# Performance work log

Measured on AMD Instinct MI355X. Metric: run time of the kernel, lower is better.

The kernel has to match this reference:

```python
import jax, jax.numpy as jnp
import numpy as np

INV_SQRT2 = 0.7071067811865476


def _dense(x, W):
    return jax.nn.silu(x @ W)


def _residual(x, Wa, Wb):
    # GemNet ResidualLayer: two activated dense layers, skip, 1/sqrt(2) rescale
    return (x + _dense(_dense(x, Wa), Wb)) * INV_SQRT2


def setup_inputs() -> dict:
    key = jax.random.key(0)
    ks = iter(jax.random.split(key, 40))
    N, E, T = 10000, 200000, 400000
    NR, NS = 128, 7          # num_radial, num_spherical
    A, M, Ti, To, C = 128, 256, 64, 64, 16
    NB = 2                   # num_blocks

    def w(shape):
        fan_in = shape[-2]
        return jax.random.normal(next(ks), shape, jnp.float32) / float(np.sqrt(fan_in))

    inp = {}
    inp['atomic_numbers'] = jax.random.randint(next(ks), (N,), 0, 120)
    inp['idx_s'] = jax.random.randint(next(ks), (E,), 0, N)
    inp['idx_t'] = jax.random.randint(next(ks), (E,), 0, N)
    inp['id3_ba'] = jax.random.randint(next(ks), (T,), 0, E)
    inp['id3_ca'] = jax.random.randint(next(ks), (T,), 0, E)
    inp['rbf'] = jax.random.uniform(next(ks), (E, NR), jnp.float32)
    inp['cbf'] = jax.random.normal(next(ks), (T, NS), jnp.float32)
    V = jax.random.normal(next(ks), (E, 3), jnp.float32)
    inp['V_st'] = V / jnp.linalg.norm(V, axis=-1, keepdims=True)
    inp['atom_table'] = jax.random.normal(next(ks), (120, A), jnp.float32)
    inp['W_edge_in'] = w((2 * A + NR, M))
    inp['rbf_w3'] = w((NB, NR, M))
    inp['W_down'] = w((NB, M, Ti))
    inp['W_cbf'] = w((NB, NS, C))
    inp['W_bil'] = jax.random.normal(next(ks), (NB, C, Ti, To), jnp.float32) / float(np.sqrt(C * Ti))
    inp['W_up'] = w((NB, To, M))
    inp['W_res_e'] = w((NB, 4, M, M))
    inp['rbf_wh'] = w((NB, NR, M))
    inp['W_e2a'] = w((NB, M, A))
    inp['W_res_a'] = w((NB, 2, A, A))
    inp['W_outE_in'] = w((A * (NB + 1), A))
    inp['W_outE_res'] = w((2, A, A))
    inp['W_outE_fin'] = w((A, 1))
    inp['W_outF_in'] = w((M * (NB + 1), M))
    inp['W_outF_res'] = w((2, M, M))
    inp['W_outF_fin'] = w((M, 1))
    return inp


def reference(atomic_numbers, idx_s, idx_t, id3_ba, id3_ca, rbf, cbf, V_st,
              atom_table, W_edge_in, rbf_w3, W_down, W_cbf, W_bil, W_up,
              W_res_e, rbf_wh, W_e2a, W_res_a,
              W_outE_in, W_outE_res, W_outE_fin,
              W_outF_in, W_outF_res, W_outF_fin):
    N = atomic_numbers.shape[0]
    E = idx_s.shape[0]
    NB = rbf_w3.shape[0]

    # atom and edge embeddings
    h = atom_table[atomic_numbers]                                       # [N, A]
    m = _dense(jnp.concatenate([h[idx_s], h[idx_t], rbf], axis=-1), W_edge_in)  # [E, M]

    xs_E = [h]
    xs_F = [m]
    for b in range(NB):
        # --- triplet interaction: edge -> triplet gather, bilinear CBF mix, scatter back ---
        x = (m * (rbf @ rbf_w3[b])) @ W_down[b]                          # [E, Ti]
        cb = cbf @ W_cbf[b]                                              # [T, C]
        y = jnp.einsum('tc,ti,cio->to', cb, x[id3_ba], W_bil[b])         # [T, To]
        agg = jax.ops.segment_sum(y, id3_ca, num_segments=E)             # [E, To]
        x3 = _dense(agg @ W_up[b], jnp.eye(x3_dim := W_up[b].shape[1], dtype=m.dtype)) if False else jax.nn.silu(agg @ W_up[b])  # [E, M]
        # --- residual / skip structure ---
        m2 = _residual(m, W_res_e[b, 0], W_res_e[b, 1])
        m2 = (m2 + x3) * INV_SQRT2
        m = _residual(m2, W_res_e[b, 2], W_res_e[b, 3])
        # --- atom update: edge -> atom scatter ---
        xa = (m * (rbf @ rbf_wh[b])) @ W_e2a[b]                          # [E, A]
        ha = jax.ops.segment_sum(xa, idx_t, num_segments=N)              # [N, A]
        h = h + _residual(ha, W_res_a[b, 0], W_res_a[b, 1])
        xs_E.append(h)
        xs_F.append(m)

    # FinalMLP-style heads over concatenated per-block features (emb*(num_blocks+1))
    xE = _residual(_dense(jnp.concatenate(xs_E, axis=-1), W_outE_in), W_outE_res[0], W_outE_res[1])
    E_atom = xE @ W_outE_fin                                             # [N, 1]
    xF = _residual(_dense(jnp.concatenate(xs_F, axis=-1), W_outF_in), W_outF_res[0], W_outF_res[1])
    F_edge = xF @ W_outF_fin                                             # [E, 1]
    forces = jax.ops.segment_sum(F_edge * V_st, idx_t, num_segments=N)   # [N, 3]
    return jnp.concatenate([E_atom, forces], axis=-1)                    # [N, 4]
```

## Files before the change

### kernel.cpp

```cpp
#include <hip/hip_runtime.h>
#include <hip/hip_bf16.h>
#include <cstdio>

#define INV2 0.70710678118654752440f
typedef __hip_bfloat16 bf16;
typedef __attribute__((ext_vector_type(8))) short short8v;
typedef __attribute__((ext_vector_type(8))) unsigned short u16x8;
typedef __attribute__((ext_vector_type(4))) float f32x4;

__device__ __forceinline__ float silu_f(float v) { return v / (1.0f + __expf(-v)); }
__device__ __forceinline__ float bf2f(unsigned short u) {
    union { unsigned int i; float f; } t; t.i = ((unsigned int)u) << 16; return t.f;
}
__device__ __forceinline__ unsigned short f2bf(float x) {
    bf16 b = __float2bfloat16(x);
    return *reinterpret_cast<unsigned short*>(&b);
}
__device__ __forceinline__ float toF(float v) { return v; }
__device__ __forceinline__ float toF(bf16 v) { return __bfloat162float(v); }
__device__ __forceinline__ void stF(float* p, float v) { *p = v; }
__device__ __forceinline__ void stF(bf16* p, float v) { *p = __float2bfloat16(v); }

__device__ __forceinline__ void ld8f(const float* p, float* o) {
    const float4 a = ((const float4*)p)[0], b = ((const float4*)p)[1];
    o[0]=a.x; o[1]=a.y; o[2]=a.z; o[3]=a.w; o[4]=b.x; o[5]=b.y; o[6]=b.z; o[7]=b.w;
}
__device__ __forceinline__ void ld8f(const bf16* p, float* o) {
    const u16x8 u = *(const u16x8*)p;
#pragma unroll
    for (int j = 0; j < 8; j++) o[j] = bf2f(u[j]);
}

__device__ __forceinline__ void gll16(const void* g, void* l) {
    __builtin_amdgcn_global_load_lds(
        (const __attribute__((address_space(1))) unsigned int*)g,
        (__attribute__((address_space(3))) unsigned int*)l, 16, 0, 0);
}

enum { AM_NORMAL = 0, AM_MUL2 = 1, AM_GATHER = 2, AM_SILU = 3, AM_DMA = 4 };
enum { EP_PLAIN = 0, EP_SILU = 1, EP_ACCUM = 2, EP_RES2 = 3, EP_RESADD = 4, EP_HEADRES = 5 };

template <int AMODE, int EPI, int BN, typename AT, typename CT>
__global__ __launch_bounds__(256) void mgemm(
    const AT* __restrict__ A, const AT* __restrict__ A2,
    const int* __restrict__ gs, const int* __restrict__ gt,
    const bf16* __restrict__ Bt,
    CT* __restrict__ C, const CT* __restrict__ X,
    int Mrows, int Ncols, int K)
{
    constexpr bool DMA = (AMODE == AM_DMA);
    constexpr int AST = DMA ? 32 : 40;
    constexpr int FM = (BN == 128) ? 4 : 2;
    __shared__ __align__(16) unsigned short Als[128 * AST];
    __shared__ __align__(16) unsigned short Bls[BN * 32];
    const int tid = threadIdx.x;
    const int row0 = blockIdx.x * 128, col0 = blockIdx.y * BN;

    const int sr = tid >> 1;
    const int sh = (tid & 1) * 16;
    const int gr = row0 + sr;
    const bool rok = (gr < Mrows);
    int is_ = 0, it_ = 0;
    if (AMODE == AM_GATHER) { if (rok) { is_ = gs[gr]; it_ = gt[gr]; } }

    const int l = tid & 63, wid = tid >> 6;
    const int lr = l & 15;
    const int lk = (l >> 4) * 8;
    const int wrow = (BN == 128) ? ((wid & 1) * 64) : (wid * 32);
    const int wcol = (BN == 128) ? ((wid >> 1) * 64) : 0;

    f32x4 acc[FM][4];
#pragma unroll
    for (int i = 0; i < FM; i++)
#pragma unroll
        for (int j = 0; j < 4; j++)
#pragma unroll
            for (int q = 0; q < 4; q++) acc[i][j][q] = 0.f;

    for (int k0 = 0; k0 < K; k0 += 32) {
        if constexpr (DMA) {
#pragma unroll
            for (int i = 0; i < 2; i++) {
                const int c = i * 256 + tid;
                const int row = c >> 2;
                if (row0 + row < Mrows)
                    gll16(A + (size_t)(row0 + row) * K + k0 + (c & 3) * 8, &Als[c * 8]);
            }
        } else {
            float va[16];
            if (rok) {
                if (AMODE == AM_GATHER) {
                    const int reg = k0 >> 7, koff = (k0 & 127) + sh;
                    const AT* src = (reg == 0) ? (A + (size_t)is_ * 128 + koff)
                                  : (reg == 1) ? (A + (size_t)it_ * 128 + koff)
                                               : (A2 + (size_t)gr * 128 + koff);
                    ld8f(src, va); ld8f(src + 8, va + 8);
                } else {
                    const AT* src = A + (size_t)gr * K + k0 + sh;
                    ld8f(src, va); ld8f(src + 8, va + 8);
                    if (AMODE == AM_MUL2) {
                        float vb[16];
                        const AT* s2 = A2 + (size_t)gr * K + k0 + sh;
                        ld8f(s2, vb); ld8f(s2 + 8, vb + 8);
#pragma unroll
                        for (int j = 0; j < 16; j++) va[j] *= vb[j];
                    } else if (AMODE == AM_SILU) {
#pragma unroll
                        for (int j = 0; j < 16; j++) va[j] = silu_f(va[j]);
                    }
                }
            } else {
#pragma unroll
                for (int j = 0; j < 16; j++) va[j] = 0.f;
            }
            u16x8 av0, av1;
#pragma unroll
            for (int j = 0; j < 8; j++) { av0[j] = f2bf(va[j]); av1[j] = f2bf(va[j + 8]); }
            *(u16x8*)&Als[sr * AST + sh] = av0;
            *(u16x8*)&Als[sr * AST + sh + 8] = av1;
        }

#pragma unroll
        for (int i = 0; i < BN / 64; i++) {
            const int c = i * 256 + tid;
            gll16(Bt + (size_t)(col0 + (c >> 2)) * K + k0 + (c & 3) * 8, &Bls[c * 8]);
        }

        __syncthreads();

        short8v af[FM], bfr[4];
#pragma unroll
        for (int fm = 0; fm < FM; fm++)
            af[fm] = *(const short8v*)&Als[(wrow + fm * 16 + lr) * AST + lk];
#pragma unroll
        for (int fn = 0; fn < 4; fn++)
            bfr[fn] = *(const short8v*)&Bls[(wcol + fn * 16 + lr) * 32 + lk];
#pragma unroll
        for (int fm = 0; fm < FM; fm++)
#pragma unroll
            for (int fn = 0; fn < 4; fn++)
                acc[fm][fn] = __builtin_amdgcn_mfma_f32_16x16x32_bf16(
                    af[fm], bfr[fn], acc[fm][fn], 0, 0, 0);

        __syncthreads();
    }

#pragma unroll
    for (int fm = 0; fm < FM; fm++) {
        const int rb = row0 + wrow + fm * 16 + (l >> 4) * 4;
#pragma unroll
        for (int fn = 0; fn < 4; fn++) {
            const int c = col0 + wcol + fn * 16 + lr;
#pragma unroll
            for (int r = 0; r < 4; r++) {
                const int rr = rb + r;
                if (rr >= Mrows) continue;
                const size_t o = (size_t)rr * Ncols + c;
                const float v = acc[fm][fn][r];
                if (EPI == EP_PLAIN)        stF(&C[o], v);
                else if (EPI == EP_SILU)    stF(&C[o], silu_f(v));
                else if (EPI == EP_ACCUM)   stF(&C[o], toF(C[o]) + v);
                else if (EPI == EP_RES2)    stF(&C[o], (toF(C[o]) + silu_f(v)) * INV2);
                else if (EPI == EP_RESADD)  stF(&C[o], toF(C[o]) + (toF(X[o]) + silu_f(v)) * INV2);
                else if (EPI == EP_HEADRES) stF(&C[o], (silu_f(toF(X[o])) + silu_f(v)) * INV2);
            }
        }
    }
}

__global__ __launch_bounds__(256) void trip_gemm(
    const bf16* __restrict__ x,
    const bf16* __restrict__ cb,
    const int* __restrict__ ba, const int* __restrict__ ca,
    const bf16* __restrict__ BtT,
    float* __restrict__ agg)
{
    __shared__ __align__(16) unsigned short At[128 * 40];
    __shared__ __align__(16) unsigned short Bs[64 * 40];
    const int tid = threadIdx.x;
    const int gr0 = blockIdx.x * 128;

    const int sr = tid >> 1, sh = tid & 1;
    const int gr = gr0 + sr;
    const int e = ba[gr];
    float xr[32];
    {
        const bf16* xp = x + (size_t)e * 64 + sh * 16;
        const u16x8 a0 = *(const u16x8*)xp;
        const u16x8 a1 = *(const u16x8*)(xp + 8);
        const u16x8 b0 = *(const u16x8*)(xp + 32);
        const u16x8 b1 = *(const u16x8*)(xp + 40);
#pragma unroll
        for (int j = 0; j < 8; j++) {
            xr[j] = bf2f(a0[j]); xr[8 + j] = bf2f(a1[j]);
            xr[16 + j] = bf2f(b0[j]); xr[24 + j] = bf2f(b1[j]);
        }
    }
    float cbr[16];
    {
        const u16x8 c0 = *(const u16x8*)(cb + (size_t)gr * 16);
        const u16x8 c1 = *(const u16x8*)(cb + (size_t)gr * 16 + 8);
#pragma unroll
// ... 40 lines not shown
#pragma unroll
            for (int fn = 0; fn < 4; fn++)
                acc[fm][fn] = __builtin_amdgcn_mfma_f32_16x16x32_bf16(
                    af[fm], bf4[fn], acc[fm][fn], 0, 0, 0);
        __syncthreads();
    }

#pragma unroll
    for (int fm = 0; fm < 2; fm++)
#pragma unroll
        for (int q = 0; q < 4; q++) {
            const int rr = wrow + fm * 16 + lg * 4 + q;
            const int eo = ca[gr0 + rr];
#pragma unroll
            for (int fn = 0; fn < 4; fn++)
                atomicAdd(&agg[(size_t)eo * 64 + fn * 16 + lr], acc[fm][fn][q]);
        }
}

__global__ __launch_bounds__(256) void cb16(const float* __restrict__ cbf,
                                            const float* __restrict__ Wcb,
                                            bf16* __restrict__ cb, int T)
{
    const int gid = blockIdx.x * 256 + threadIdx.x;
    const int t = gid >> 4, c = gid & 15;
    if (t >= T) return;
    const float* cr = cbf + (size_t)t * 7;
    float s = 0.f;
#pragma unroll
    for (int k = 0; k < 7; k++) s += cr[k] * Wcb[k * 16 + c];
    cb[(size_t)t * 16 + c] = __float2bfloat16(s);
}

struct TJob { const float* src; bf16* dst; int K; int N; };
struct TJobs { TJob j[40]; };

__global__ __launch_bounds__(256) void transpose_weights(TJobs JB) {
    const TJob J = JB.j[blockIdx.y];
    const int total = J.K * J.N;
    const int gid = blockIdx.x * 256 + threadIdx.x;
    if (gid >= total) return;
    const int n = gid / J.K, k = gid - n * J.K;
    J.dst[(size_t)n * J.K + k] = __float2bfloat16(J.src[(size_t)k * J.N + n]);
}

__global__ __launch_bounds__(256) void embed_h(const int* __restrict__ z,
                                               const float* __restrict__ tab,
                                               float* __restrict__ h, int N)
{
    const int gid = blockIdx.x * 256 + threadIdx.x;
    const int n = gid >> 7, j = gid & 127;
    if (n >= N) return;
    h[(size_t)n * 128 + j] = tab[(size_t)z[n] * 128 + j];
}

__global__ __launch_bounds__(256) void scatter_ha(const bf16* __restrict__ xa,
                                                  const int* __restrict__ idxt,
                                                  float* __restrict__ ha, int E)
{
    const int gid = blockIdx.x * 256 + threadIdx.x;
    const int e = gid >> 7, j = gid & 127;
    if (e >= E) return;
    atomicAdd(&ha[(size_t)idxt[e] * 128 + j], toF(xa[(size_t)e * 128 + j]));
}

template <typename AT>
__global__ __launch_bounds__(256) void rowdot(const AT* __restrict__ Xm,
                                              const float* __restrict__ w,
                                              float* __restrict__ outv,
                                              int rows, int width, int ostride)
{
    const int wid = (blockIdx.x * 256 + threadIdx.x) >> 6;
    const int lane = threadIdx.x & 63;
    if (wid >= rows) return;
    float s = 0.f;
    for (int q = lane; q < width; q += 64) s += toF(Xm[(size_t)wid * width + q]) * w[q];
#pragma unroll
    for (int off = 32; off > 0; off >>= 1) s += __shfl_down(s, off);
    if (lane == 0) outv[(size_t)wid * ostride] = s;
}

__global__ __launch_bounds__(256) void scatter_forces(const float* __restrict__ Fe,
                                                      const float* __restrict__ Vst,
                                                      const int* __restrict__ idxt,
                                                      float* __restrict__ out, int E)
{
    const int e = blockIdx.x * 256 + threadIdx.x;
    if (e >= E) return;
    const float f = Fe[e];
    const int n = idxt[e];
    atomicAdd(&out[(size_t)n * 4 + 1], f * Vst[(size_t)e * 3 + 0]);
    atomicAdd(&out[(size_t)n * 4 + 2], f * Vst[(size_t)e * 3 + 1]);
    atomicAdd(&out[(size_t)n * 4 + 3], f * Vst[(size_t)e * 3 + 2]);
}

#define MG(AM, EP, BNv, Aptr, A2p, GS, GT, Btp, Cp, Xp, MR, NC, KK)                       \
    mgemm<AM, EP, BNv><<<dim3(((MR) + 127) / 128, (NC) / (BNv)), 256, 0, stream>>>(       \
        Aptr, A2p, GS, GT, Btp, Cp, Xp, MR, NC, KK)

extern "C" void kernel_launch(void* const* d_in, const int* in_sizes, int n_in,
                              void* d_out, int out_size, void* d_ws, size_t ws_size,
                              hipStream_t stream)
{
    const int N = in_sizes[0];
    const int E = in_sizes[1];
    const int T = in_sizes[3];
    const int NB = 2;

    const int*   z        = (const int*)d_in[0];
    const int*   idx_s    = (const int*)d_in[1];
    const int*   idx_t    = (const int*)d_in[2];
    const int*   id3_ba   = (const int*)d_in[3];
    const int*   id3_ca   = (const int*)d_in[4];
    const float* rbf      = (const float*)d_in[5];
    const float* cbf      = (const float*)d_in[6];
    const float* V_st     = (const float*)d_in[7];
    const float* atom_tab = (const float*)d_in[8];
    const float* W_edge_in= (const float*)d_in[9];
    const float* rbf_w3   = (const float*)d_in[10];
    const float* W_down   = (const float*)d_in[11];
    const float* W_cbf    = (const float*)d_in[12];
    const float* W_bil    = (const float*)d_in[13];
    const float* W_up     = (const float*)d_in[14];
    const float* W_res_e  = (const float*)d_in[15];
    const float* rbf_wh   = (const float*)d_in[16];
    const float* W_e2a    = (const float*)d_in[17];
    const float* W_res_a  = (const float*)d_in[18];
    const float* W_outE_in  = (const float*)d_in[19];
    const float* W_outE_res = (const float*)d_in[20];
    const float* W_outE_fin = (const float*)d_in[21];
    const float* W_outF_in  = (const float*)d_in[22];
// ... 14 lines not shown
    float* headE = (float*)alloc((size_t)N * 128 * 4);
    float* ha    = (float*)alloc((size_t)N * 128 * 4);
    float* tA    = (float*)alloc((size_t)N * 128 * 4);
    bf16 *bt_outF[3], *bt_outE[3], *bt_r3[2], *bt_down[2], *bt_bilT[2], *bt_up[2],
         *bt_rese[8], *bt_rh[2], *bt_e2a[2], *bt_resa[4], *bt_Fres[2], *bt_Eres[2];
    bf16* bt_edge = (bf16*)alloc(384 * 256 * 2);
    for (int s = 0; s < 3; s++) bt_outF[s] = (bf16*)alloc(256 * 256 * 2);
    for (int s = 0; s < 3; s++) bt_outE[s] = (bf16*)alloc(128 * 128 * 2);
    for (int b = 0; b < 2; b++) bt_r3[b]   = (bf16*)alloc(256 * 128 * 2);
    for (int b = 0; b < 2; b++) bt_down[b] = (bf16*)alloc(64 * 256 * 2);
    for (int b = 0; b < 2; b++) bt_bilT[b] = (bf16*)alloc(64 * 1024 * 2);
    for (int b = 0; b < 2; b++) bt_up[b]   = (bf16*)alloc(256 * 64 * 2);
    for (int i = 0; i < 8; i++) bt_rese[i] = (bf16*)alloc(256 * 256 * 2);
    for (int b = 0; b < 2; b++) bt_rh[b]   = (bf16*)alloc(256 * 128 * 2);
    for (int b = 0; b < 2; b++) bt_e2a[b]  = (bf16*)alloc(128 * 256 * 2);
    for (int i = 0; i < 4; i++) bt_resa[i] = (bf16*)alloc(128 * 128 * 2);
    for (int i = 0; i < 2; i++) bt_Fres[i] = (bf16*)alloc(256 * 256 * 2);
    for (int i = 0; i < 2; i++) bt_Eres[i] = (bf16*)alloc(128 * 128 * 2);
    if (off > ws_size) {
        fprintf(stderr, "kernel_launch: ws too small: need %zu have %zu\n", off, ws_size);
        return;
    }
    bf16*  xa = (bf16*)agg;
    float* Fe = (float*)xbuf;
    float* xE = ha;
    bf16*  cbS = S1;

    const float* nfp = nullptr;
    const bf16*  nbp = nullptr;
    const int*   nip = nullptr;

    {
        TJobs JB; int nj = 0;
        auto addj = [&](const float* s, bf16* d, int K, int Nn) { JB.j[nj++] = TJob{s, d, K, Nn}; };
        addj(W_edge_in, bt_edge, 384, 256);
        for (int s = 0; s < 3; s++) addj(W_outF_in + (size_t)s * 256 * 256, bt_outF[s], 256, 256);
        for (int s = 0; s < 3; s++) addj(W_outE_in + (size_t)s * 128 * 128, bt_outE[s], 128, 128);
        for (int b = 0; b < 2; b++) addj(rbf_w3 + (size_t)b * 128 * 256, bt_r3[b], 128, 256);
        for (int b = 0; b < 2; b++) addj(W_down + (size_t)b * 256 * 64, bt_down[b], 256, 64);
        for (int b = 0; b < 2; b++) addj(W_bil + (size_t)b * 65536, bt_bilT[b], 1024, 64);
        for (int b = 0; b < 2; b++) addj(W_up + (size_t)b * 64 * 256, bt_up[b], 64, 256);
        for (int i = 0; i < 8; i++) addj(W_res_e + (size_t)i * 65536, bt_rese[i], 256, 256);
        for (int b = 0; b < 2; b++) addj(rbf_wh + (size_t)b * 128 * 256, bt_rh[b], 128, 256);
        for (int b = 0; b < 2; b++) addj(W_e2a + (size_t)b * 256 * 128, bt_e2a[b], 256, 128);
        for (int i = 0; i < 4; i++) addj(W_res_a + (size_t)i * 16384, bt_resa[i], 128, 128);
        for (int i = 0; i < 2; i++) addj(W_outF_res + (size_t)i * 65536, bt_Fres[i], 256, 256);
        for (int i = 0; i < 2; i++) addj(W_outE_res + (size_t)i * 16384, bt_Eres[i], 128, 128);
        transpose_weights<<<dim3(384, nj), 256, 0, stream>>>(JB);
    }

    embed_h<<<(N * 128 + 255) / 256, 256, 0, stream>>>(z, atom_tab, h_cur, N);
    MG(AM_GATHER, EP_SILU, 128, h_cur, rbf, idx_s, idx_t, bt_edge, m_cur, nbp, E, 256, 384);
    MG(AM_DMA, EP_PLAIN, 128, m_cur, nbp, nip, nip, bt_outF[0], headF, nbp, E, 256, 256);
    MG(AM_NORMAL, EP_PLAIN, 64, h_cur, nfp, nip, nip, bt_outE[0], headE, nfp, N, 128, 128);

    for (int b = 0; b < NB; ++b) {
        const float* Wcb = W_cbf + (size_t)b * 7 * 16;

        MG(AM_NORMAL, EP_PLAIN, 128, rbf, nfp, nip, nip, bt_r3[b], S1, nbp, E, 256, 128);
        MG(AM_MUL2, EP_PLAIN, 64, m_cur, S1, nip, nip, bt_down[b], xbuf, nbp, E, 64, 256);
        cb16<<<(T * 16 + 255) / 256, 256, 0, stream>>>(cbf, Wcb, cbS, T);
        (void)hipMemsetAsync(agg, 0, (size_t)E * 64 * sizeof(float), stream);
        trip_gemm<<<T / 128, 256, 0, stream>>>(xbuf, cbS, id3_ba, id3_ca, bt_bilT[b], agg);

        MG(AM_DMA, EP_SILU, 128, m_cur, nbp, nip, nip, bt_rese[4 * b + 0], S1, nbp, E, 256, 256);
        MG(AM_DMA, EP_RES2, 128, S1, nbp, nip, nip, bt_rese[4 * b + 1], m_cur, nbp, E, 256, 256);
        MG(AM_NORMAL, EP_RES2, 128, agg, nfp, nip, nip, bt_up[b], m_cur, nbp, E, 256, 64);
        MG(AM_DMA, EP_SILU, 128, m_cur, nbp, nip, nip, bt_rese[4 * b + 2], S1, nbp, E, 256, 256);
        MG(AM_DMA, EP_RES2, 128, S1, nbp, nip, nip, bt_rese[4 * b + 3], m_cur, nbp, E, 256, 256);
        MG(AM_DMA, EP_ACCUM, 128, m_cur, nbp, nip, nip, bt_outF[b + 1], headF, nbp, E, 256, 256);

        MG(AM_NORMAL, EP_PLAIN, 128, rbf, nfp, nip, nip, bt_rh[b], S1, nbp, E, 256, 128);
        MG(AM_MUL2, EP_PLAIN, 128, m_cur, S1, nip, nip, bt_e2a[b], xa, nbp, E, 128, 256);
        (void)hipMemsetAsync(ha, 0, (size_t)N * 128 * sizeof(float), stream);
        scatter_ha<<<(E * 128 + 255) / 256, 256, 0, stream>>>(xa, idx_t, ha, E);
        MG(AM_NORMAL, EP_SILU, 64, ha, nfp, nip, nip, bt_resa[2 * b + 0], tA, nfp, N, 128, 128);
        MG(AM_NORMAL, EP_RESADD, 64, tA, nfp, nip, nip, bt_resa[2 * b + 1], h_cur, ha, N, 128, 128);
        MG(AM_NORMAL, EP_ACCUM, 64, h_cur, nfp, nip, nip, bt_outE[b + 1], headE, nfp, N, 128, 128);
    }

    MG(AM_SILU, EP_SILU, 128, headF, nbp, nip, nip, bt_Fres[0], S1, nbp, E, 256, 256);
    MG(AM_DMA, EP_HEADRES, 128, S1, nbp, nip, nip, bt_Fres[1], m_cur, headF, E, 256, 256);
    rowdot<<<(E * 64 + 255) / 256, 256, 0, stream>>>(m_cur, W_outF_fin, Fe, E, 256, 1);

    (void)hipMemsetAsync(out, 0, (size_t)out_size * sizeof(float), stream);
    MG(AM_SILU, EP_SILU, 64, headE, nfp, nip, nip, bt_Eres[0], tA, nfp, N, 128, 128);
    MG(AM_NORMAL, EP_HEADRES, 64, tA, nfp, nip, nip, bt_Eres[1], xE, headE, N, 128, 128);
    rowdot<<<(N * 64 + 255) / 256, 256, 0, stream>>>(xE, W_outE_fin, out, N, 128, 4);
    scatter_forces<<<(E + 255) / 256, 256, 0, stream>>>(Fe, V_st, idx_t, out, E);
}
```

Baseline: 2.891 ms.

## Replace tiled GEMM with whole-K weight-resident kernel loading A fragments directly

The generic GEMM is rewritten so each workgroup loads the full-K slice of a 64-column weight tile into shared memory once. A fragments are then read straight from global memory into registers, with no A staging in LDS and no per-K-step barriers. The K loop is fully unrolled via a template parameter, and blocks are remapped across XCDs with a chunked ID swizzle so that neighbouring tiles land on the same XCD. In exchange, output tiles are narrower (64 columns), so the A rows are re-read once per column tile, and the direct loads may be less coalesced than the old DMA path.

```diff
diff --git a/kernel.cpp b/kernel.cpp
--- a/kernel.cpp
+++ b/kernel.cpp
@@ -25,138 +25,146 @@
     const float4 a = ((const float4*)p)[0], b = ((const float4*)p)[1];
     o[0]=a.x; o[1]=a.y; o[2]=a.z; o[3]=a.w; o[4]=b.x; o[5]=b.y; o[6]=b.z; o[7]=b.w;
 }
-__device__ __forceinline__ void ld8f(const bf16* p, float* o) {
-    const u16x8 u = *(const u16x8*)p;
-#pragma unroll
-    for (int j = 0; j < 8; j++) o[j] = bf2f(u[j]);
-}
-
-__device__ __forceinline__ void gll16(const void* g, void* l) {
-    __builtin_amdgcn_global_load_lds(
-        (const __attribute__((address_space(1))) unsigned int*)g,
-        (__attribute__((address_space(3))) unsigned int*)l, 16, 0, 0);
-}
-
-enum { AM_NORMAL = 0, AM_MUL2 = 1, AM_GATHER = 2, AM_SILU = 3, AM_DMA = 4 };
+__device__ __forceinline__ short8v pack8(const float* va) {
+    short8v r;
+#pragma unroll
+    for (int j = 0; j < 8; j++) r[j] = (short)f2bf(va[j]);
+    return r;
+}
+
+enum { AM_NORMAL = 0, AM_MUL2 = 1, AM_GATHER = 2, AM_SILU = 3 };
 enum { EP_PLAIN = 0, EP_SILU = 1, EP_ACCUM = 2, EP_RES2 = 3, EP_RESADD = 4, EP_HEADRES = 5 };
 
-template <int AMODE, int EPI, int BN, typename AT, typename CT>
-__global__ __launch_bounds__(256) void mgemm(
+template <int AMODE, int KK, typename AT>
+__device__ __forceinline__ short8v afrag(const AT* __restrict__ A,
+                                         const AT* __restrict__ A2,
+                                         const int* __restrict__ gs,
+                                         const int* __restrict__ gt,
+                                         int row, int k0, int lk)
+{
+    if constexpr (AMODE == AM_GATHER) {
+        const int reg = k0 >> 7, ko = (k0 & 127) + lk;
+        const float* src = (reg == 0) ? (const float*)A + (size_t)gs[row] * 128 + ko
+                         : (reg == 1) ? (const float*)A + (size_t)gt[row] * 128 + ko
+                                      : (const float*)A2 + (size_t)row * 128 + ko;
+        float va[8]; ld8f(src, va);
+        return pack8(va);
+    } else if constexpr (sizeof(AT) == 2) {
+        const u16x8 u = *(const u16x8*)((const bf16*)A + (size_t)row * KK + k0 + lk);
+        if constexpr (AMODE == AM_NORMAL) {
+            short8v r;
+#pragma unroll
+            for (int j = 0; j < 8; j++) r[j] = (short)u[j];
+            return r;
+        } else if constexpr (AMODE == AM_SILU) {
+            float va[8];
+#pragma unroll
+            for (int j = 0; j < 8; j++) va[j] = silu_f(bf2f(u[j]));
+            return pack8(va);
+        } else {
+            const u16x8 v = *(const u16x8*)((const bf16*)A2 + (size_t)row * KK + k0 + lk);
+            float va[8];
+#pragma unroll
+            for (int j = 0; j < 8; j++) va[j] = bf2f(u[j]) * bf2f(v[j]);
+            return pack8(va);
+        }
+    } else {
+        float va[8];
+        ld8f((const float*)A + (size_t)row * KK + k0 + lk, va);
+        if constexpr (AMODE == AM_SILU) {
+#pragma unroll
+            for (int j = 0; j < 8; j++) va[j] = silu_f(va[j]);
+        } else if constexpr (AMODE == AM_MUL2) {
+            float vb[8];
+            ld8f((const float*)A2 + (size_t)row * KK + k0 + lk, vb);
+#pragma unroll
+            for (int j = 0; j < 8; j++) va[j] *= vb[j];
+        }
+        return pack8(va);
+    }
+}
+
+template <int AMODE, int EPI, int KK, typename AT, typename CT>
+__global__ __launch_bounds__(256) void wgemm(
     const AT* __restrict__ A, const AT* __restrict__ A2,
     const int* __restrict__ gs, const int* __restrict__ gt,
     const bf16* __restrict__ Bt,
     CT* __restrict__ C, const CT* __restrict__ X,
-    int Mrows, int Ncols, int K)
-{
-    constexpr bool DMA = (AMODE == AM_DMA);
-    constexpr int AST = DMA ? 32 : 40;
-    constexpr int FM = (BN == 128) ? 4 : 2;
-    __shared__ __align__(16) unsigned short Als[128 * AST];
-    __shared__ __align__(16) unsigned short Bls[BN * 32];
+    int Mrows, int Ncols)
+{
+    constexpr int KP = KK + 8;
+    __shared__ __align__(16) unsigned short Bls[64 * KP];
     const int tid = threadIdx.x;
-    const int row0 = blockIdx.x * 128, col0 = blockIdx.y * BN;
-
-    const int sr = tid >> 1;
-    const int sh = (tid & 1) * 16;
-    const int gr = row0 + sr;
-    const bool rok = (gr < Mrows);
-    int is_ = 0, it_ = 0;
-    if (AMODE == AM_GATHER) { if (rok) { is_ = gs[gr]; it_ = gt[gr]; } }
-
-    const int l = tid & 63, wid = tid >> 6;
-    const int lr = l & 15;
-    const int lk = (l >> 4) * 8;
-    const int wrow = (BN == 128) ? ((wid & 1) * 64) : (wid * 32);
-    const int wcol = (BN == 128) ? ((wid >> 1) * 64) : 0;
-
-    f32x4 acc[FM][4];
-#pragma unroll
-    for (int i = 0; i < FM; i++)
+
+    const int nwg = gridDim.x;
+    int id = blockIdx.x;
+    if (nwg >= 8) {
+        const int q = nwg >> 3, r = nwg & 7, x = id & 7, lid = id >> 3;
+        id = (x < r ? x * (q + 1) : r * (q + 1) + (x - r) * q) + lid;
+    }
+    const int gy = Ncols >> 6;
+    const int col0 = (id % gy) * 64;
+    const int row0 = (id / gy) * 128;
+
+    constexpr int NCH = 64 * (KK / 8);
+#pragma unroll
+    for (int i = 0; i < (NCH + 255) / 256; i++) {
+        const int c = i * 256 + tid;
+        if (NCH % 256 == 0 || c < NCH) {
+            const int bc = c / (KK / 8), ch = c % (KK / 8);
+            *(u16x8*)&Bls[bc * KP + ch * 8] =
+                *(const u16x8*)(Bt + (size_t)(col0 + bc) * KK + ch * 8);
+        }
+    }
+    __syncthreads();
+
+    const int l = tid & 63, wv = tid >> 6;
+    const int lr = l & 15, lg = l >> 4, lk = lg * 8;
+    const int wrow = wv * 32;
+
+    const int r0 = row0 + wrow + lr;
+    const int r1 = r0 + 16;
+    const bool ok0 = r0 < Mrows, ok1 = r1 < Mrows;
+
+    f32x4 acc[2][4];
+#pragma unroll
+    for (int i = 0; i < 2; i++)
 #pragma unroll
         for (int j = 0; j < 4; j++)
 #pragma unroll
             for (int q = 0; q < 4; q++) acc[i][j][q] = 0.f;
 
-    for (int k0 = 0; k0 < K; k0 += 32) {
-        if constexpr (DMA) {
-#pragma unroll
-            for (int i = 0; i < 2; i++) {
-                const int c = i * 256 + tid;
-                const int row = c >> 2;
-                if (row0 + row < Mrows)
-                    gll16(A + (size_t)(row0 + row) * K + k0 + (c & 3) * 8, &Als[c * 8]);
-            }
-        } else {
-            float va[16];
-            if (rok) {
-                if (AMODE == AM_GATHER) {
-                    const int reg = k0 >> 7, koff = (k0 & 127) + sh;
-                    const AT* src = (reg == 0) ? (A + (size_t)is_ * 128 + koff)
-                                  : (reg == 1) ? (A + (size_t)it_ * 128 + koff)
-                                               : (A2 + (size_t)gr * 128 + koff);
-                    ld8f(src, va); ld8f(src + 8, va + 8);
-                } else {
-                    const AT* src = A + (size_t)gr * K + k0 + sh;
-                    ld8f(src, va); ld8f(src + 8, va + 8);
-                    if (AMODE == AM_MUL2) {
-                        float vb[16];
-                        const AT* s2 = A2 + (size_t)gr * K + k0 + sh;
-                        ld8f(s2, vb); ld8f(s2 + 8, vb + 8);
-#pragma unroll
-                        for (int j = 0; j < 16; j++) va[j] *= vb[j];
-                    } else if (AMODE == AM_SILU) {
-#pragma unroll
-                        for (int j = 0; j < 16; j++) va[j] = silu_f(va[j]);
-                    }
-                }
-            } else {
-#pragma unroll
-                for (int j = 0; j < 16; j++) va[j] = 0.f;
-            }
-            u16x8 av0, av1;
-#pragma unroll
-            for (int j = 0; j < 8; j++) { av0[j] = f2bf(va[j]); av1[j] = f2bf(va[j + 8]); }
-            *(u16x8*)&Als[sr * AST + sh] = av0;
-            *(u16x8*)&Als[sr * AST + sh + 8] = av1;
-        }
-
-#pragma unroll
-        for (int i = 0; i < BN / 64; i++) {
-            const int c = i * 256 + tid;
-            gll16(Bt + (size_t)(col0 + (c >> 2)) * K + k0 + (c & 3) * 8, &Bls[c * 8]);
-        }
-
-        __syncthreads();
-
-        short8v af[FM], bfr[4];
-#pragma unroll
-        for (int fm = 0; fm < FM; fm++)
-            af[fm] = *(const short8v*)&Als[(wrow + fm * 16 + lr) * AST + lk];
+    short8v zf;
+#pragma unroll
+    for (int j = 0; j < 8; j++) zf[j] = 0;
+
+#pragma unroll
+    for (int k0 = 0; k0 < KK; k0 += 32) {
+        const short8v a0 = ok0 ? afrag<AMODE, KK>(A, A2, gs, gt, r0, k0, lk) : zf;
+        const short8v a1 = ok1 ? afrag<AMODE, KK>(A, A2, gs, gt, r1, k0, lk) : zf;
+        short8v bf4[4];
 #pragma unroll
         for (int fn = 0; fn < 4; fn++)
-            bfr[fn] = *(const short8v*)&Bls[(wcol + fn * 16 + lr) * 32 + lk];
-#pragma unroll
-        for (int fm = 0; fm < FM; fm++)
-#pragma unroll
-            for (int fn = 0; fn < 4; fn++)
-                acc[fm][fn] = __builtin_amdgcn_mfma_f32_16x16x32_bf16(
-                    af[fm], bfr[fn], acc[fm][fn], 0, 0, 0);
-
-        __syncthreads();
-    }
-
-#pragma unroll
-    for (int fm = 0; fm < FM; fm++) {
-        const int rb = row0 + wrow + fm * 16 + (l >> 4) * 4;
+            bf4[fn] = *(const short8v*)&Bls[(fn * 16 + lr) * KP + k0 + lk];
 #pragma unroll
         for (int fn = 0; fn < 4; fn++) {
-            const int c = col0 + wcol + fn * 16 + lr;
-#pragma unroll
-            for (int r = 0; r < 4; r++) {
-                const int rr = rb + r;
+            acc[0][fn] = __builtin_amdgcn_mfma_f32_16x16x32_bf16(a0, bf4[fn], acc[0][fn], 0, 0, 0);
+            acc[1][fn] = __builtin_amdgcn_mfma_f32_16x16x32_bf16(a1, bf4[fn], acc[1][fn], 0, 0, 0);
+        }
+    }
+
+#pragma unroll
+    for (int fm = 0; fm < 2; fm++) {
+        const int rb = row0 + wrow + fm * 16 + lg * 4;
+#pragma unroll
+        for (int fn = 0; fn < 4; fn++) {
+            const int c = col0 + fn * 16 + lr;
+#pragma unroll
+            for (int q = 0; q < 4; q++) {
+                const int rr = rb + q;
                 if (rr >= Mrows) continue;
                 const size_t o = (size_t)rr * Ncols + c;
-                const float v = acc[fm][fn][r];
+                const float v = acc[fm][fn][q];
                 if (EPI == EP_PLAIN)        stF(&C[o], v);
                 else if (EPI == EP_SILU)    stF(&C[o], silu_f(v));
                 else if (EPI == EP_ACCUM)   stF(&C[o], toF(C[o]) + v);
@@ -336,9 +344,9 @@
     atomicAdd(&out[(size_t)n * 4 + 3], f * Vst[(size_t)e * 3 + 2]);
 }
 
-#define MG(AM, EP, BNv, Aptr, A2p, GS, GT, Btp, Cp, Xp, MR, NC, KK)                       \
-    mgemm<AM, EP, BNv><<<dim3(((MR) + 127) / 128, (NC) / (BNv)), 256, 0, stream>>>(       \
-        Aptr, A2p, GS, GT, Btp, Cp, Xp, MR, NC, KK)
+#define WG(AM, EP, KKv, Aptr, A2p, GS, GT, Btp, Cp, Xp, MR, NC)                            \
+    wgemm<AM, EP, KKv><<<(((MR) + 127) / 128) * ((NC) / 64), 256, 0, stream>>>(            \
+        Aptr, A2p, GS, GT, Btp, Cp, Xp, MR, NC)
 
 extern "C" void kernel_launch(void* const* d_in, const int* in_sizes, int n_in,
                               void* d_out, int out_size, void* d_ws, size_t ws_size,
@@ -437,42 +445,42 @@
     }
 
     embed_h<<<(N * 128 + 255) / 256, 256, 0, stream>>>(z, atom_tab, h_cur, N);
-    MG(AM_GATHER, EP_SILU, 128, h_cur, rbf, idx_s, idx_t, bt_edge, m_cur, nbp, E, 256, 384);
-    MG(AM_DMA, EP_PLAIN, 128, m_cur, nbp, nip, nip, bt_outF[0], headF, nbp, E, 256, 256);
-    MG(AM_NORMAL, EP_PLAIN, 64, h_cur, nfp, nip, nip, bt_outE[0], headE, nfp, N, 128, 128);
+    WG(AM_GATHER, EP_SILU, 384, h_cur, rbf, idx_s, idx_t, bt_edge, m_cur, nbp, E, 256);
+    WG(AM_NORMAL, EP_PLAIN, 256, m_cur, nbp, nip, nip, bt_outF[0], headF, nbp, E, 256);
+    WG(AM_NORMAL, EP_PLAIN, 128, h_cur, nfp, nip, nip, bt_outE[0], headE, nfp, N, 128);
 
     for (int b = 0; b < NB; ++b) {
         const float* Wcb = W_cbf + (size_t)b * 7 * 16;
 
-        MG(AM_NORMAL, EP_PLAIN, 128, rbf, nfp, nip, nip, bt_r3[b], S1, nbp, E, 256, 128);
-        MG(AM_MUL2, EP_PLAIN, 64, m_cur, S1, nip, nip, bt_down[b], xbuf, nbp, E, 64, 256);
+        WG(AM_NORMAL, EP_PLAIN, 128, rbf, nfp, nip, nip, bt_r3[b], S1, nbp, E, 256);
+        WG(AM_MUL2, EP_PLAIN, 256, m_cur, S1, nip, nip, bt_down[b], xbuf, nbp, E, 64);
         cb16<<<(T * 16 + 255) / 256, 256, 0, stream>>>(cbf, Wcb, cbS, T);
         (void)hipMemsetAsync(agg, 0, (size_t)E * 64 * sizeof(float), stream);
         trip_gemm<<<T / 128, 256, 0, stream>>>(xbuf, cbS, id3_ba, id3_ca, bt_bilT[b], agg);
 
-        MG(AM_DMA, EP_SILU, 128, m_cur, nbp, nip, nip, bt_rese[4 * b + 0], S1, nbp, E, 256, 256);
-        MG(AM_DMA, EP_RES2, 128, S1, nbp, nip, nip, bt_rese[4 * b + 1], m_cur, nbp, E, 256, 256);
-        MG(AM_NORMAL, EP_RES2, 128, agg, nfp, nip, nip, bt_up[b], m_cur, nbp, E, 256, 64);
-        MG(AM_DMA, EP_SILU, 128, m_cur, nbp, nip, nip, bt_rese[4 * b + 2], S1, nbp, E, 256, 256);
-        MG(AM_DMA, EP_RES2, 128, S1, nbp, nip, nip, bt_rese[4 * b + 3], m_cur, nbp, E, 256, 256);
-        MG(AM_DMA, EP_ACCUM, 128, m_cur, nbp, nip, nip, bt_outF[b + 1], headF, nbp, E, 256, 256);
-
-        MG(AM_NORMAL, EP_PLAIN, 128, rbf, nfp, nip, nip, bt_rh[b], S1, nbp, E, 256, 128);
-        MG(AM_MUL2, EP_PLAIN, 128, m_cur, S1, nip, nip, bt_e2a[b], xa, nbp, E, 128, 256);
+        WG(AM_NORMAL, EP_SILU, 256, m_cur, nbp, nip, nip, bt_rese[4 * b + 0], S1, nbp, E, 256);
+        WG(AM_NORMAL, EP_RES2, 256, S1, nbp, nip, nip, bt_rese[4 * b + 1], m_cur, nbp, E, 256);
+        WG(AM_NORMAL, EP_RES2, 64, agg, nfp, nip, nip, bt_up[b], m_cur, nbp, E, 256);
+        WG(AM_NORMAL, EP_SILU, 256, m_cur, nbp, nip, nip, bt_rese[4 * b + 2], S1, nbp, E, 256);
+        WG(AM_NORMAL, EP_RES2, 256, S1, nbp, nip, nip, bt_rese[4 * b + 3], m_cur, nbp, E, 256);
+        WG(AM_NORMAL, EP_ACCUM, 256, m_cur, nbp, nip, nip, bt_outF[b + 1], headF, nbp, E, 256);
+
+        WG(AM_NORMAL, EP_PLAIN, 128, rbf, nfp, nip, nip, bt_rh[b], S1, nbp, E, 256);
+        WG(AM_MUL2, EP_PLAIN, 256, m_cur, S1, nip, nip, bt_e2a[b], xa, nbp, E, 128);
         (void)hipMemsetAsync(ha, 0, (size_t)N * 128 * sizeof(float), stream);
         scatter_ha<<<(E * 128 + 255) / 256, 256, 0, stream>>>(xa, idx_t, ha, E);
-        MG(AM_NORMAL, EP_SILU, 64, ha, nfp, nip, nip, bt_resa[2 * b + 0], tA, nfp, N, 128, 128);
-        MG(AM_NORMAL, EP_RESADD, 64, tA, nfp, nip, nip, bt_resa[2 * b + 1], h_cur, ha, N, 128, 128);
-        MG(AM_NORMAL, EP_ACCUM, 64, h_cur, nfp, nip, nip, bt_outE[b + 1], headE, nfp, N, 128, 128);
-    }
-
-    MG(AM_SILU, EP_SILU, 128, headF, nbp, nip, nip, bt_Fres[0], S1, nbp, E, 256, 256);
-    MG(AM_DMA, EP_HEADRES, 128, S1, nbp, nip, nip, bt_Fres[1], m_cur, headF, E, 256, 256);
+        WG(AM_NORMAL, EP_SILU, 128, ha, nfp, nip, nip, bt_resa[2 * b + 0], tA, nfp, N, 128);
+        WG(AM_NORMAL, EP_RESADD, 128, tA, nfp, nip, nip, bt_resa[2 * b + 1], h_cur, ha, N, 128);
+        WG(AM_NORMAL, EP_ACCUM, 128, h_cur, nfp, nip, nip, bt_outE[b + 1], headE, nfp, N, 128);
+    }
+
+    WG(AM_SILU, EP_SILU, 256, headF, nbp, nip, nip, bt_Fres[0], S1, nbp, E, 256);
+    WG(AM_NORMAL, EP_HEADRES, 256, S1, nbp, nip, nip, bt_Fres[1], m_cur, headF, E, 256);
     rowdot<<<(E * 64 + 255) / 256, 256, 0, stream>>>(m_cur, W_outF_fin, Fe, E, 256, 1);
 
     (void)hipMemsetAsync(out, 0, (size_t)out_size * sizeof(float), stream);
-    MG(AM_SILU, EP_SILU, 64, headE, nfp, nip, nip, bt_Eres[0], tA, nfp, N, 128, 128);
-    MG(AM_NORMAL, EP_HEADRES, 64, tA, nfp, nip, nip, bt_Eres[1], xE, headE, N, 128, 128);
+    WG(AM_SILU, EP_SILU, 128, headE, nfp, nip, nip, bt_Eres[0], tA, nfp, N, 128);
+    WG(AM_NORMAL, EP_HEADRES, 128, tA, nfp, nip, nip, bt_Eres[1], xE, headE, N, 128);
     rowdot<<<(N * 64 + 255) / 256, 256, 0, stream>>>(xE, W_outE_fin, out, N, 128, 4);
     scatter_forces<<<(E + 255) / 256, 256, 0, stream>>>(Fe, V_st, idx_t, out, E);
 }
```

After: 3.053 ms. 1.06x slower.

## Double-buffer LDS tiles in mgemm to overlap next-k loads with MFMA

Applied to the files above, without the earlier changes.

Gives the A and B shared-memory tiles two buffers each. The loads for the next k-step (register loads for A, async global-to-LDS for B) are issued before the current step's MFMAs, so global memory latency is hidden behind compute, and one of the two __syncthreads per iteration is removed. The cost is twice the LDS footprint, which may lower occupancy, plus extra registers to hold the prefetched A values.

```diff
diff --git a/kernel.cpp b/kernel.cpp
--- a/kernel.cpp
+++ b/kernel.cpp
@@ -39,6 +39,38 @@
 
 enum { AM_NORMAL = 0, AM_MUL2 = 1, AM_GATHER = 2, AM_SILU = 3, AM_DMA = 4 };
 enum { EP_PLAIN = 0, EP_SILU = 1, EP_ACCUM = 2, EP_RES2 = 3, EP_RESADD = 4, EP_HEADRES = 5 };
+
+template <int AMODE, typename AT>
+__device__ __forceinline__ void loadAreg(const AT* __restrict__ A, const AT* __restrict__ A2,
+                                         int is_, int it_, int gr, bool rok,
+                                         int K, int k0, int sh, float* va)
+{
+    if (!rok) {
+#pragma unroll
+        for (int j = 0; j < 16; j++) va[j] = 0.f;
+        return;
+    }
+    if constexpr (AMODE == AM_GATHER) {
+        const int reg = k0 >> 7, koff = (k0 & 127) + sh;
+        const AT* src = (reg == 0) ? (A + (size_t)is_ * 128 + koff)
+                      : (reg == 1) ? (A + (size_t)it_ * 128 + koff)
+                                   : (A2 + (size_t)gr * 128 + koff);
+        ld8f(src, va); ld8f(src + 8, va + 8);
+    } else {
+        const AT* src = A + (size_t)gr * K + k0 + sh;
+        ld8f(src, va); ld8f(src + 8, va + 8);
+        if constexpr (AMODE == AM_MUL2) {
+            float vb[16];
+            const AT* s2 = A2 + (size_t)gr * K + k0 + sh;
+            ld8f(s2, vb); ld8f(s2 + 8, vb + 8);
+#pragma unroll
+            for (int j = 0; j < 16; j++) va[j] *= vb[j];
+        } else if constexpr (AMODE == AM_SILU) {
+#pragma unroll
+            for (int j = 0; j < 16; j++) va[j] = silu_f(va[j]);
+        }
+    }
+}
 
 template <int AMODE, int EPI, int BN, typename AT, typename CT>
 __global__ __launch_bounds__(256) void mgemm(
@@ -51,8 +83,8 @@
     constexpr bool DMA = (AMODE == AM_DMA);
     constexpr int AST = DMA ? 32 : 40;
     constexpr int FM = (BN == 128) ? 4 : 2;
-    __shared__ __align__(16) unsigned short Als[128 * AST];
-    __shared__ __align__(16) unsigned short Bls[BN * 32];
+    __shared__ __align__(16) unsigned short Als[2][128 * AST];
+    __shared__ __align__(16) unsigned short Bls[2][BN * 32];
     const int tid = threadIdx.x;
     const int row0 = blockIdx.x * 128, col0 = blockIdx.y * BN;
 
@@ -77,64 +109,62 @@
 #pragma unroll
             for (int q = 0; q < 4; q++) acc[i][j][q] = 0.f;
 
-    for (int k0 = 0; k0 < K; k0 += 32) {
-        if constexpr (DMA) {
-#pragma unroll
-            for (int i = 0; i < 2; i++) {
-                const int c = i * 256 + tid;
-                const int row = c >> 2;
-                if (row0 + row < Mrows)
-                    gll16(A + (size_t)(row0 + row) * K + k0 + (c & 3) * 8, &Als[c * 8]);
-            }
-        } else {
-            float va[16];
-            if (rok) {
-                if (AMODE == AM_GATHER) {
-                    const int reg = k0 >> 7, koff = (k0 & 127) + sh;
-                    const AT* src = (reg == 0) ? (A + (size_t)is_ * 128 + koff)
-                                  : (reg == 1) ? (A + (size_t)it_ * 128 + koff)
-                                               : (A2 + (size_t)gr * 128 + koff);
-                    ld8f(src, va); ld8f(src + 8, va + 8);
-                } else {
-                    const AT* src = A + (size_t)gr * K + k0 + sh;
-                    ld8f(src, va); ld8f(src + 8, va + 8);
-                    if (AMODE == AM_MUL2) {
-                        float vb[16];
-                        const AT* s2 = A2 + (size_t)gr * K + k0 + sh;
-                        ld8f(s2, vb); ld8f(s2 + 8, vb + 8);
-#pragma unroll
-                        for (int j = 0; j < 16; j++) va[j] *= vb[j];
-                    } else if (AMODE == AM_SILU) {
-#pragma unroll
-                        for (int j = 0; j < 16; j++) va[j] = silu_f(va[j]);
-                    }
+    if constexpr (DMA) {
+#pragma unroll
+        for (int i = 0; i < 2; i++) {
+            const int c = i * 256 + tid, row = c >> 2;
+            if (row0 + row < Mrows)
+                gll16(A + (size_t)(row0 + row) * K + (c & 3) * 8, &Als[0][c * 8]);
+        }
+    } else {
+        float v0[16];
+        loadAreg<AMODE>(A, A2, is_, it_, gr, rok, K, 0, sh, v0);
+        u16x8 av0, av1;
+#pragma unroll
+        for (int j = 0; j < 8; j++) { av0[j] = f2bf(v0[j]); av1[j] = f2bf(v0[j + 8]); }
+        *(u16x8*)&Als[0][sr * AST + sh] = av0;
+        *(u16x8*)&Als[0][sr * AST + sh + 8] = av1;
+    }
+#pragma unroll
+    for (int i = 0; i < BN / 64; i++) {
+        const int c = i * 256 + tid;
+        gll16(Bt + (size_t)(col0 + (c >> 2)) * K + (c & 3) * 8, &Bls[0][c * 8]);
+    }
+
+    int cur = 0;
+    for (int k0 = 0; ; k0 += 32) {
+        __syncthreads();
+
+        const int kn = k0 + 32;
+        const bool more = kn < K;
+        const int nb = cur ^ 1;
+
+        float vnext[16];
+        if (more) {
+            if constexpr (DMA) {
+#pragma unroll
+                for (int i = 0; i < 2; i++) {
+                    const int c = i * 256 + tid, row = c >> 2;
+                    if (row0 + row < Mrows)
+                        gll16(A + (size_t)(row0 + row) * K + kn + (c & 3) * 8, &Als[nb][c * 8]);
                 }
             } else {
-#pragma unroll
-                for (int j = 0; j < 16; j++) va[j] = 0.f;
+                loadAreg<AMODE>(A, A2, is_, it_, gr, rok, K, kn, sh, vnext);
             }
-            u16x8 av0, av1;
-#pragma unroll
-            for (int j = 0; j < 8; j++) { av0[j] = f2bf(va[j]); av1[j] = f2bf(va[j + 8]); }
-            *(u16x8*)&Als[sr * AST + sh] = av0;
-            *(u16x8*)&Als[sr * AST + sh + 8] = av1;
-        }
-
-#pragma unroll
-        for (int i = 0; i < BN / 64; i++) {
-            const int c = i * 256 + tid;
-            gll16(Bt + (size_t)(col0 + (c >> 2)) * K + k0 + (c & 3) * 8, &Bls[c * 8]);
-        }
-
-        __syncthreads();
+#pragma unroll
+            for (int i = 0; i < BN / 64; i++) {
+                const int c = i * 256 + tid;
+                gll16(Bt + (size_t)(col0 + (c >> 2)) * K + kn + (c & 3) * 8, &Bls[nb][c * 8]);
+            }
+        }
 
         short8v af[FM], bfr[4];
 #pragma unroll
         for (int fm = 0; fm < FM; fm++)
-            af[fm] = *(const short8v*)&Als[(wrow + fm * 16 + lr) * AST + lk];
+            af[fm] = *(const short8v*)&Als[cur][(wrow + fm * 16 + lr) * AST + lk];
 #pragma unroll
         for (int fn = 0; fn < 4; fn++)
-            bfr[fn] = *(const short8v*)&Bls[(wcol + fn * 16 + lr) * 32 + lk];
+            bfr[fn] = *(const short8v*)&Bls[cur][(wcol + fn * 16 + lr) * 32 + lk];
 #pragma unroll
         for (int fm = 0; fm < FM; fm++)
 #pragma unroll
@@ -142,7 +172,18 @@
                 acc[fm][fn] = __builtin_amdgcn_mfma_f32_16x16x32_bf16(
                     af[fm], bfr[fn], acc[fm][fn], 0, 0, 0);
 
-        __syncthreads();
+        if constexpr (!DMA) {
+            if (more) {
+                u16x8 av0, av1;
+#pragma unroll
+                for (int j = 0; j < 8; j++) { av0[j] = f2bf(vnext[j]); av1[j] = f2bf(vnext[j + 8]); }
+                *(u16x8*)&Als[nb][sr * AST + sh] = av0;
+                *(u16x8*)&Als[nb][sr * AST + sh + 8] = av1;
+            }
+        }
+
+        if (!more) break;
+        cur = nb;
     }
 
 #pragma unroll
```

Result: slower. 3.046 ms (+5.3%).

## Add specialized 256x256 bf16 GEMM with resident swizzled weight tile in LDS

Applied to the files above, without the earlier changes.

Adds a dedicated pgemm kernel for the E×256×256 bf16 GEMMs. It keeps half of the 128-column weight tile resident in LDS (reloaded once at the K midpoint) and double-buffers the A tiles through direct global-to-LDS loads with explicit vmcnt waits. Weights used by these GEMMs are pre-swizzled during the transpose so LDS reads avoid bank conflicts. The large LDS footprint (about 48KB) may limit occupancy, and the swizzle must match exactly between the transpose and the kernel.

```diff
diff --git a/kernel.cpp b/kernel.cpp
--- a/kernel.cpp
+++ b/kernel.cpp
@@ -168,6 +168,104 @@
     }
 }
 
+template <int EPI>
+__global__ __launch_bounds__(256) void pgemm(
+    const bf16* __restrict__ A, const bf16* __restrict__ Bt,
+    bf16* __restrict__ C, const bf16* __restrict__ X, int Mrows)
+{
+    __shared__ __align__(16) unsigned short Bls[128 * 128];
+    __shared__ __align__(16) unsigned short Als[2][4096];
+    const int tid = threadIdx.x;
+    const int row0 = blockIdx.x * 128, col0 = blockIdx.y * 128;
+    const int l = tid & 63, wv = tid >> 6;
+    const int lr = l & 15, lg = l >> 4, lk = lg * 8;
+
+    f32x4 acc[2][8];
+#pragma unroll
+    for (int i = 0; i < 2; i++)
+#pragma unroll
+        for (int j = 0; j < 8; j++)
+#pragma unroll
+            for (int q = 0; q < 4; q++) acc[i][j][q] = 0.f;
+
+    auto stageA = [&](int buf, int k0) {
+#pragma unroll
+        for (int j = 0; j < 2; j++) {
+            const int c = j * 64 + l;
+            const int row = c >> 2, koff = (c & 3) * 8;
+            const int rowg = row0 + wv * 32 + row;
+            if (rowg < Mrows)
+                gll16(A + (size_t)rowg * 256 + k0 + (koff ^ ((row & 3) << 3)),
+                      &Als[buf][wv * 1024 + c * 8]);
+        }
+    };
+    auto stageB = [&](int kh) {
+#pragma unroll
+        for (int i = 0; i < 8; i++) {
+            const int c = i * 256 + tid;
+            const int bc = c >> 4, ch = c & 15;
+            gll16(Bt + (size_t)(col0 + bc) * 256 + kh * 128 + ch * 8, &Bls[c * 8]);
+        }
+    };
+
+    stageB(0);
+    stageA(0, 0);
+    __syncthreads();
+
+#pragma unroll
+    for (int s = 0; s < 8; s++) {
+        if (s == 4) {
+            __syncthreads();
+            stageB(1);
+            __syncthreads();
+        }
+        const bool more = (s < 7);
+        if (more) stageA((s & 1) ^ 1, (s + 1) * 32);
+        __builtin_amdgcn_sched_barrier(0);
+        if (more) asm volatile("s_waitcnt vmcnt(2)" ::: "memory");
+        else      asm volatile("s_waitcnt vmcnt(0)" ::: "memory");
+        __builtin_amdgcn_sched_barrier(0);
+
+        const int cur = s & 1;
+        const int kb = (s & 3) * 32;
+        const unsigned short* Aw = &Als[cur][wv * 1024];
+        const short8v a0 = *(const short8v*)&Aw[lr * 32 + (lk ^ ((lr & 3) << 3))];
+        const short8v a1 = *(const short8v*)&Aw[(lr + 16) * 32 + (lk ^ ((lr & 3) << 3))];
+        short8v bf8[8];
+#pragma unroll
+        for (int fn = 0; fn < 8; fn++) {
+            const int cc = fn * 16 + lr;
+            bf8[fn] = *(const short8v*)&Bls[cc * 128 + ((kb + lk) ^ ((cc & 7) << 3))];
+        }
+#pragma unroll
+        for (int fn = 0; fn < 8; fn++) {
+            acc[0][fn] = __builtin_amdgcn_mfma_f32_16x16x32_bf16(a0, bf8[fn], acc[0][fn], 0, 0, 0);
+            acc[1][fn] = __builtin_amdgcn_mfma_f32_16x16x32_bf16(a1, bf8[fn], acc[1][fn], 0, 0, 0);
+        }
+    }
+
+#pragma unroll
+    for (int fm = 0; fm < 2; fm++) {
+        const int rb = row0 + wv * 32 + fm * 16 + lg * 4;
+#pragma unroll
+        for (int fn = 0; fn < 8; fn++) {
+            const int c = col0 + fn * 16 + lr;
+#pragma unroll
+            for (int q = 0; q < 4; q++) {
+                const int rr = rb + q;
+                if (rr >= Mrows) continue;
+                const size_t o = (size_t)rr * 256 + c;
+                const float v = acc[fm][fn][q];
+                if (EPI == EP_PLAIN)        stF(&C[o], v);
+                else if (EPI == EP_SILU)    stF(&C[o], silu_f(v));
+                else if (EPI == EP_ACCUM)   stF(&C[o], toF(C[o]) + v);
+                else if (EPI == EP_RES2)    stF(&C[o], (toF(C[o]) + silu_f(v)) * INV2);
+                else if (EPI == EP_HEADRES) stF(&C[o], (silu_f(toF(X[o])) + silu_f(v)) * INV2);
+            }
+        }
+    }
+}
+
 __global__ __launch_bounds__(256) void trip_gemm(
     const bf16* __restrict__ x,
     const bf16* __restrict__ cb,
@@ -274,7 +372,7 @@
     cb[(size_t)t * 16 + c] = __float2bfloat16(s);
 }
 
-struct TJob { const float* src; bf16* dst; int K; int N; };
+struct TJob { const float* src; bf16* dst; int K; int N; int swz; };
 struct TJobs { TJob j[40]; };
 
 __global__ __launch_bounds__(256) void transpose_weights(TJobs JB) {
@@ -283,7 +381,8 @@
     const int gid = blockIdx.x * 256 + threadIdx.x;
     if (gid >= total) return;
     const int n = gid / J.K, k = gid - n * J.K;
-    J.dst[(size_t)n * J.K + k] = __float2bfloat16(J.src[(size_t)k * J.N + n]);
+    const int pos = J.swz ? (k ^ ((n & 7) << 3)) : k;
+    J.dst[(size_t)n * J.K + pos] = __float2bfloat16(J.src[(size_t)k * J.N + n]);
 }
 
 __global__ __launch_bounds__(256) void embed_h(const int* __restrict__ z,
@@ -339,6 +438,9 @@
 #define MG(AM, EP, BNv, Aptr, A2p, GS, GT, Btp, Cp, Xp, MR, NC, KK)                       \
     mgemm<AM, EP, BNv><<<dim3(((MR) + 127) / 128, (NC) / (BNv)), 256, 0, stream>>>(       \
         Aptr, A2p, GS, GT, Btp, Cp, Xp, MR, NC, KK)
+
+#define PG(EP, Aptr, Btp, Cp, Xp, MR)                                                     \
+    pgemm<EP><<<dim3(((MR) + 127) / 128, 2), 256, 0, stream>>>(Aptr, Btp, Cp, Xp, MR)
 
 extern "C" void kernel_launch(void* const* d_in, const int* in_sizes, int n_in,
                               void* d_out, int out_size, void* d_ws, size_t ws_size,
@@ -419,26 +521,29 @@
 
     {
         TJobs JB; int nj = 0;
-        auto addj = [&](const float* s, bf16* d, int K, int Nn) { JB.j[nj++] = TJob{s, d, K, Nn}; };
-        addj(W_edge_in, bt_edge, 384, 256);
-        for (int s = 0; s < 3; s++) addj(W_outF_in + (size_t)s * 256 * 256, bt_outF[s], 256, 256);
-        for (int s = 0; s < 3; s++) addj(W_outE_in + (size_t)s * 128 * 128, bt_outE[s], 128, 128);
-        for (int b = 0; b < 2; b++) addj(rbf_w3 + (size_t)b * 128 * 256, bt_r3[b], 128, 256);
-        for (int b = 0; b < 2; b++) addj(W_down + (size_t)b * 256 * 64, bt_down[b], 256, 64);
-        for (int b = 0; b < 2; b++) addj(W_bil + (size_t)b * 65536, bt_bilT[b], 1024, 64);
-        for (int b = 0; b < 2; b++) addj(W_up + (size_t)b * 64 * 256, bt_up[b], 64, 256);
-        for (int i = 0; i < 8; i++) addj(W_res_e + (size_t)i * 65536, bt_rese[i], 256, 256);
-        for (int b = 0; b < 2; b++) addj(rbf_wh + (size_t)b * 128 * 256, bt_rh[b], 128, 256);
-        for (int b = 0; b < 2; b++) addj(W_e2a + (size_t)b * 256 * 128, bt_e2a[b], 256, 128);
-        for (int i = 0; i < 4; i++) addj(W_res_a + (size_t)i * 16384, bt_resa[i], 128, 128);
-        for (int i = 0; i < 2; i++) addj(W_outF_res + (size_t)i * 65536, bt_Fres[i], 256, 256);
-        for (int i = 0; i < 2; i++) addj(W_outE_res + (size_t)i * 16384, bt_Eres[i], 128, 128);
+        auto addj = [&](const float* s, bf16* d, int K, int Nn, int swz) {
+            JB.j[nj++] = TJob{s, d, K, Nn, swz};
+        };
+        addj(W_edge_in, bt_edge, 384, 256, 0);
+        for (int s = 0; s < 3; s++) addj(W_outF_in + (size_t)s * 256 * 256, bt_outF[s], 256, 256, 1);
+        for (int s = 0; s < 3; s++) addj(W_outE_in + (size_t)s * 128 * 128, bt_outE[s], 128, 128, 0);
+        for (int b = 0; b < 2; b++) addj(rbf_w3 + (size_t)b * 128 * 256, bt_r3[b], 128, 256, 0);
+        for (int b = 0; b < 2; b++) addj(W_down + (size_t)b * 256 * 64, bt_down[b], 256, 64, 0);
+        for (int b = 0; b < 2; b++) addj(W_bil + (size_t)b * 65536, bt_bilT[b], 1024, 64, 0);
+        for (int b = 0; b < 2; b++) addj(W_up + (size_t)b * 64 * 256, bt_up[b], 64, 256, 0);
+        for (int i = 0; i < 8; i++) addj(W_res_e + (size_t)i * 65536, bt_rese[i], 256, 256, 1);
+        for (int b = 0; b < 2; b++) addj(rbf_wh + (size_t)b * 128 * 256, bt_rh[b], 128, 256, 0);
+        for (int b = 0; b < 2; b++) addj(W_e2a + (size_t)b * 256 * 128, bt_e2a[b], 256, 128, 0);
+        for (int i = 0; i < 4; i++) addj(W_res_a + (size_t)i * 16384, bt_resa[i], 128, 128, 0);
+        addj(W_outF_res, bt_Fres[0], 256, 256, 0);
+        addj(W_outF_res + 65536, bt_Fres[1], 256, 256, 1);
+        for (int i = 0; i < 2; i++) addj(W_outE_res + (size_t)i * 16384, bt_Eres[i], 128, 128, 0);
         transpose_weights<<<dim3(384, nj), 256, 0, stream>>>(JB);
     }
 
     embed_h<<<(N * 128 + 255) / 256, 256, 0, stream>>>(z, atom_tab, h_cur, N);
     MG(AM_GATHER, EP_SILU, 128, h_cur, rbf, idx_s, idx_t, bt_edge, m_cur, nbp, E, 256, 384);
-    MG(AM_DMA, EP_PLAIN, 128, m_cur, nbp, nip, nip, bt_outF[0], headF, nbp, E, 256, 256);
+    PG(EP_PLAIN, m_cur, bt_outF[0], headF, nbp, E);
     MG(AM_NORMAL, EP_PLAIN, 64, h_cur, nfp, nip, nip, bt_outE[0], headE, nfp, N, 128, 128);
 
     for (int b = 0; b < NB; ++b) {
@@ -450,12 +555,12 @@
         (void)hipMemsetAsync(agg, 0, (size_t)E * 64 * sizeof(float), stream);
         trip_gemm<<<T / 128, 256, 0, stream>>>(xbuf, cbS, id3_ba, id3_ca, bt_bilT[b], agg);
 
-        MG(AM_DMA, EP_SILU, 128, m_cur, nbp, nip, nip, bt_rese[4 * b + 0], S1, nbp, E, 256, 256);
-        MG(AM_DMA, EP_RES2, 128, S1, nbp, nip, nip, bt_rese[4 * b + 1], m_cur, nbp, E, 256, 256);
+        PG(EP_SILU, m_cur, bt_rese[4 * b + 0], S1, nbp, E);
+        PG(EP_RES2, S1, bt_rese[4 * b + 1], m_cur, nbp, E);
         MG(AM_NORMAL, EP_RES2, 128, agg, nfp, nip, nip, bt_up[b], m_cur, nbp, E, 256, 64);
-        MG(AM_DMA, EP_SILU, 128, m_cur, nbp, nip, nip, bt_rese[4 * b + 2], S1, nbp, E, 256, 256);
-        MG(AM_DMA, EP_RES2, 128, S1, nbp, nip, nip, bt_rese[4 * b + 3], m_cur, nbp, E, 256, 256);
-        MG(AM_DMA, EP_ACCUM, 128, m_cur, nbp, nip, nip, bt_outF[b + 1], headF, nbp, E, 256, 256);
+        PG(EP_SILU, m_cur, bt_rese[4 * b + 2], S1, nbp, E);
+        PG(EP_RES2, S1, bt_rese[4 * b + 3], m_cur, nbp, E);
+        PG(EP_ACCUM, m_cur, bt_outF[b + 1], headF, nbp, E);
 
         MG(AM_NORMAL, EP_PLAIN, 128, rbf, nfp, nip, nip, bt_rh[b], S1, nbp, E, 256, 128);
         MG(AM_MUL2, EP_PLAIN, 128, m_cur, S1, nip, nip, bt_e2a[b], xa, nbp, E, 128, 256);
@@ -467,7 +572,7 @@
     }
 
     MG(AM_SILU, EP_SILU, 128, headF, nbp, nip, nip, bt_Fres[0], S1, nbp, E, 256, 256);
-    MG(AM_DMA, EP_HEADRES, 128, S1, nbp, nip, nip, bt_Fres[1], m_cur, headF, E, 256, 256);
+    PG(EP_HEADRES, S1, bt_Fres[1], m_cur, headF, E);
     rowdot<<<(E * 64 + 255) / 256, 256, 0, stream>>>(m_cur, W_outF_fin, Fe, E, 256, 1);
 
     (void)hipMemsetAsync(out, 0, (size_t)out_size * sizeof(float), stream);
```

Result: slower. 3.114 ms (+7.7%).
